# Optimization experiments

Measured on AMD Instinct MI355X. Metric: run time of the kernel, lower is better.

## Reference

```python
import jax, jax.numpy as jnp
import numpy as np

N_NODES = 100000


def gcn_conv(x, W, b, src, dst, n_nodes):
    """PyG-style GCNConv: out = D^{-1/2} (A + I) D^{-1/2} (x @ W) + b."""
    h = x @ W  # [N, F_out] transform first (smaller message dim)
    # add self-loops
    loops = jnp.arange(n_nodes, dtype=src.dtype)
    s = jnp.concatenate([src, loops])
    d = jnp.concatenate([dst, loops])
    # symmetric normalization
    deg = jnp.zeros((n_nodes,), dtype=h.dtype).at[d].add(1.0)
    dinv = jnp.where(deg > 0, jax.lax.rsqrt(deg), 0.0)
    norm = dinv[s] * dinv[d]  # [E+N]
    msg = h[s] * norm[:, None]  # gather from sources
    out = jax.ops.segment_sum(msg, d, num_segments=n_nodes)  # scatter-add at targets
    return out + b


def setup_inputs() -> dict:
    key = jax.random.key(0)
    k1, k2, k3, k4 = jax.random.split(key, 4)
    in_ch, hid, out_ch = 128, 75, 40
    n_edges = 3200000
    x = jax.random.normal(k1, (N_NODES, in_ch), dtype=jnp.float32)
    edge_index = jax.random.randint(k2, (2, n_edges), 0, N_NODES, dtype=jnp.int64)
    # Glorot-style init for GCNConv weights, zero bias (PyG default)
    W1 = jax.random.normal(k3, (in_ch, hid), dtype=jnp.float32) * (1.0 / np.sqrt(in_ch))
    b1 = jnp.zeros((hid,), dtype=jnp.float32)
    W2 = jax.random.normal(k4, (hid, out_ch), dtype=jnp.float32) * (1.0 / np.sqrt(hid))
    b2 = jnp.zeros((out_ch,), dtype=jnp.float32)
    return {"x": x, "edge_index": edge_index, "W1": W1, "b1": b1, "W2": W2, "b2": b2}


def reference(x, edge_index, W1, b1, W2, b2):
    src, dst = edge_index[0], edge_index[1]
    h = gcn_conv(x, W1, b1, src, dst, N_NODES)
    h = jax.nn.relu(h)
    h = gcn_conv(h, W2, b2, src, dst, N_NODES)
    return jax.nn.log_softmax(h, axis=1)
```

## Files before the change

### kernel.cpp

```cpp
#include <hip/hip_runtime.h>

#define N_NODES 100000
#define IN_CH 128
#define HID 75
#define OUT_CH 40
#define N_EDGES 3200000

#define NB 196
#define CAP 20000
#define EPT 16
#define PA_EDGES (EPT * 256)

typedef unsigned short u16;
typedef unsigned int u32;
typedef unsigned char u8;
typedef short short8 __attribute__((ext_vector_type(8)));
typedef float f32x4 __attribute__((ext_vector_type(4)));
typedef float f32x2 __attribute__((ext_vector_type(2)));
typedef u32 u32x2 __attribute__((ext_vector_type(2)));
typedef u32 u32x4 __attribute__((ext_vector_type(4)));

__device__ __forceinline__ u16 f2bf(float f) {
    u32 b = __float_as_uint(f);
    b += 0x7FFF + ((b >> 16) & 1);
    return (u16)(b >> 16);
}

#if __has_builtin(__builtin_amdgcn_cvt_pk_f32_fp8) && __has_builtin(__builtin_amdgcn_cvt_pk_fp8_f32)
#define HW_FP8 1
#else
#define HW_FP8 0
#endif

__device__ __forceinline__ float dec1_sw(u32 v) {
    u32 s = (v & 0x80u) << 24;
    u32 em = v & 0x7Fu;
    float mag = (em >= 8u) ? __uint_as_float((em << 20) + (120u << 23))
                           : (float)em * 0.001953125f;
    return __uint_as_float(s | __float_as_uint(mag));
}
template <int HI>
__device__ __forceinline__ f32x2 dec2(u32 w) {
#if HW_FP8
    return __builtin_amdgcn_cvt_pk_f32_fp8(w, HI);
#else
    f32x2 r;
    r.x = dec1_sw((w >> (HI * 16)) & 0xFFu);
    r.y = dec1_sw((w >> (HI * 16 + 8)) & 0xFFu);
    return r;
#endif
}
__device__ __forceinline__ u32 enc1(float f) {
#if HW_FP8
    return __builtin_amdgcn_cvt_pk_fp8_f32(f, f, 0u, false) & 0xFFu;
#else
    float cf = fminf(fmaxf(f, -448.f), 448.f);
    u32 b = __float_as_uint(cf);
    u32 sign = (b >> 24) & 0x80u;
    float af = fabsf(cf);
    if (af < 0.015625f) {
        u32 d = (u32)__builtin_rintf(af * 512.f);
        return sign | d;
    }
    u32 e = (b >> 23) & 0xFFu;
    u32 m = b & 0x7FFFFFu;
    u32 m8 = m >> 20;
    u32 rem = m & 0xFFFFFu;
    m8 += (rem > 0x80000u) || (rem == 0x80000u && (m8 & 1u));
    u32 ee = e - 120u;
    if (m8 == 8u) { m8 = 0u; ee += 1u; }
    if (ee > 15u || (ee == 15u && m8 == 7u)) { ee = 15u; m8 = 6u; }
    return sign | (ee << 3) | m8;
#endif
}

__global__ void probe64(const int* __restrict__ e, int* __restrict__ flag) {
    __shared__ int nonzero;
    if (threadIdx.x == 0) nonzero = 0;
    __syncthreads();
    int idx = threadIdx.x * 12497;
    if (e[2 * idx + 1] != 0) nonzero = 1;
    __syncthreads();
    if (threadIdx.x == 0) *flag = (nonzero == 0) ? 1 : 0;
}

__global__ __launch_bounds__(256) void init_misc(int* __restrict__ bucketCursor,
        u32* __restrict__ h1b32) {
    int i = blockIdx.x * 256 + threadIdx.x;
    if (i < NB * 16) bucketCursor[i] = 0;
    if (i < 800000) {
        int node = i >> 3, q = i & 7;
        h1b32[node * 48 + 40 + q] = 0;
    }
}

__global__ __launch_bounds__(256) void passA(const int* __restrict__ e,
        const int* __restrict__ flag, int* __restrict__ bucketCursor,
        unsigned* __restrict__ bucketBuf) {
    __shared__ int cnt[NB];
    __shared__ int base[NB];
    int t = threadIdx.x;
    for (int i = t; i < NB; i += 256) cnt[i] = 0;
    __syncthreads();
    bool w64 = (*flag != 0);
    int s_[EPT], d_[EPT];
    int eb = blockIdx.x * PA_EDGES + t;
#pragma unroll
    for (int k = 0; k < EPT; ++k) {
        int idx = eb + k * 256;
        int s = 0, d = -1;
        if (idx < N_EDGES) {
            if (w64) { s = e[2 * idx]; d = e[2 * (N_EDGES + idx)]; }
            else     { s = e[idx];     d = e[N_EDGES + idx]; }
            atomicAdd(&cnt[d >> 9], 1);
        }
        s_[k] = s; d_[k] = d;
    }
    __syncthreads();
    for (int i = t; i < NB; i += 256) {
        int c = cnt[i];
        base[i] = (c > 0) ? atomicAdd(&bucketCursor[i * 16], c) : 0;
        cnt[i] = 0;
    }
    __syncthreads();
#pragma unroll
    for (int k = 0; k < EPT; ++k) {
        int d = d_[k];
        if (d >= 0) {
            int b = d >> 9;
            int off = atomicAdd(&cnt[b], 1);
            int pos = base[b] + off;
            if (pos < CAP)
                bucketBuf[(size_t)b * CAP + pos] =
                    ((unsigned)(d & 511) << 17) | (unsigned)s_[k];
        }
    }
}

__global__ __launch_bounds__(256) void scan196(const int* __restrict__ bucketCursor,
        int* __restrict__ bucketStart, int* __restrict__ rowStart) {
    __shared__ int a[256], b[256];
    int t = threadIdx.x;
    int v = (t < NB) ? bucketCursor[t * 16] : 0;
    a[t] = v;
    __syncthreads();
    int* pin = a; int* pout = b;
    for (int o = 1; o < 256; o <<= 1) {
        int nv = pin[t] + ((t >= o) ? pin[t - o] : 0);
        pout[t] = nv;
        __syncthreads();
        int* tmp = pin; pin = pout; pout = tmp;
    }
    if (t < NB) bucketStart[t] = pin[t] - v;
    if (t == 0) rowStart[N_NODES] = N_EDGES;
}

__global__ __launch_bounds__(1024) void passB(const unsigned* __restrict__ bucketBuf,
        const int* __restrict__ bucketCursor, const int* __restrict__ bucketStart,
        int* __restrict__ csrSrc, int* __restrict__ rowStart, float* __restrict__ dinv) {
    __shared__ int cnt[512];
    __shared__ int sa[512], sb[512];
    int b = blockIdx.x;
    int t = threadIdx.x;
    int n = bucketCursor[b * 16];
    int start = bucketStart[b];
    if (t < 512) cnt[t] = 0;
    __syncthreads();
    const unsigned* buf = bucketBuf + (size_t)b * CAP;
    for (int i = t; i < n; i += 1024) atomicAdd(&cnt[buf[i] >> 17], 1);
    __syncthreads();
    if (t < 512) sa[t] = cnt[t];
    __syncthreads();
    int* pin = sa; int* pout = sb;
    for (int o = 1; o < 512; o <<= 1) {
        if (t < 512) pout[t] = pin[t] + ((t >= o) ? pin[t - o] : 0);
        __syncthreads();
        int* tmp = pin; pin = pout; pout = tmp;
    }
    int excl = 0;
    if (t < 512) {
        int deg = cnt[t];
        excl = pin[t] - deg;
        int node = b * 512 + t;
        if (node < N_NODES) {
            rowStart[node] = start + excl;
            dinv[node] = rsqrtf((float)deg + 1.0f);
        }
    }
    __syncthreads();
    if (t < 512) cnt[t] = excl;
    __syncthreads();
    for (int i = t; i < n; i += 1024) {
        unsigned p = buf[i];
        int pos = atomicAdd(&cnt[p >> 17], 1);
        csrSrc[start + pos] = (int)(p & 0x1FFFF);
    }
}

__global__ __launch_bounds__(256) void prep_w(const float* __restrict__ W1,
        const float* __restrict__ W2, u16* __restrict__ w1t, u16* __restrict__ w2t) {
    int g = blockIdx.x * 256 + threadIdx.x;
    int stride = gridDim.x * 256;
    for (int i = g; i < 80 * 128; i += stride) {
        int c = i >> 7, k = i & 127;
        w1t[i] = (c < HID) ? f2bf(W1[k * HID + c]) : (u16)0;
    }
    for (int i = g; i < 48 * 96; i += stride) {
        int c = i / 96, k = i - c * 96;
        w2t[i] = (c < OUT_CH && k < HID) ? f2bf(W2[k * OUT_CH + c]) : (u16)0;
    }
}

__global__ __launch_bounds__(256) void gemm1_mfma(const float* __restrict__ x,
        const u16* __restrict__ w1t, const float* __restrict__ dinv,
        u8* __restrict__ hsA8, u8* __restrict__ hsB8) {
    __shared__ u16 Wl[80 * 136];
    int t = threadIdx.x;
    {
        const u32* ws = (const u32*)w1t;
        u32* wd = (u32*)Wl;
        for (int i = t; i < 80 * 64; i += 256) {
            int r = i >> 6, c = i & 63;
            wd[r * 68 + c] = ws[i];
        }
    }
    __syncthreads();
    int wid = t >> 6, lane = t & 63;
    int bl = lane & 15, kh = lane >> 4;
    int row0 = blockIdx.x * 64 + wid * 16;
    short8 bf[5][4];
#pragma unroll
    for (int ct = 0; ct < 5; ++ct)
#pragma unroll
        for (int ks = 0; ks < 4; ++ks)
            bf[ct][ks] = *(const short8*)&Wl[(ct * 16 + bl) * 136 + ks * 32 + kh * 8];
    f32x4 zero = {0.f, 0.f, 0.f, 0.f};
    f32x4 acc[5];
#pragma unroll
    for (int ct = 0; ct < 5; ++ct) acc[ct] = zero;
    int arow = row0 + bl;
    bool av = (arow < N_NODES);
    const float* xr = x + (size_t)arow * IN_CH + kh * 8;
#pragma unroll
    for (int ks = 0; ks < 4; ++ks) {
        short8 af = {0, 0, 0, 0, 0, 0, 0, 0};
        if (av) {
            float4 lo = *(const float4*)(xr + ks * 32);
            float4 hi = *(const float4*)(xr + ks * 32 + 4);
            af[0] = (short)f2bf(lo.x); af[1] = (short)f2bf(lo.y);
            af[2] = (short)f2bf(lo.z); af[3] = (short)f2bf(lo.w);
            af[4] = (short)f2bf(hi.x); af[5] = (short)f2bf(hi.y);
            af[6] = (short)f2bf(hi.z); af[7] = (short)f2bf(hi.w);
        }
#pragma unroll
        for (int ct = 0; ct < 5; ++ct)
            acc[ct] = __builtin_amdgcn_mfma_f32_16x16x32_bf16(af, bf[ct][ks], acc[ct], 0, 0, 0);
    }
    int orow = row0 + kh * 4;
    float dn[4];
#pragma unroll
    for (int i = 0; i < 4; ++i)
        dn[i] = (orow + i < N_NODES) ? dinv[orow + i] * 8.f : 0.f;
#pragma unroll
    for (int ct = 0; ct < 5; ++ct) {
        int col = ct * 16 + bl;
#pragma unroll
        for (int i = 0; i < 4; ++i) {
            int r = orow + i;
            if (r < N_NODES) {
                u8 q8 = (u8)enc1(acc[ct][i] * dn[i]);
                if (ct < 4) hsA8[(size_t)r * 64 + col] = q8;
                else        hsB8[(size_t)r * 16 + (col - 64)] = q8;
            }
        }
    }
}

__global__ __launch_bounds__(256) void gemm2_mfma(const u16* __restrict__ h1b,
        const u16* __restrict__ w2t, const float* __restrict__ dinv,
        u8* __restrict__ hs2P) {
    __shared__ u16 Wl[48 * 104];
    int t = threadIdx.x;
    {
        const u32* ws = (const u32*)w2t;
        u32* wd = (u32*)Wl;
        for (int i = t; i < 48 * 48; i += 256) {
            int r = i / 48, c = i - r * 48;
            wd[r * 52 + c] = ws[i];
        }
    }
    __syncthreads();
    int wid = t >> 6, lane = t & 63;
    int bl = lane & 15, kh = lane >> 4;
    int row0 = blockIdx.x * 64 + wid * 16;
    short8 bf[3][3];
#pragma unroll
    for (int ct = 0; ct < 3; ++ct)
#pragma unroll
        for (int ks = 0; ks < 3; ++ks)
            bf[ct][ks] = *(const short8*)&Wl[(ct * 16 + bl) * 104 + ks * 32 + kh * 8];
    f32x4 zero = {0.f, 0.f, 0.f, 0.f};
    f32x4 acc[3];
#pragma unroll
    for (int ct = 0; ct < 3; ++ct) acc[ct] = zero;
    int arow = row0 + bl;
    bool av = (arow < N_NODES);
    const u16* hr = h1b + (size_t)arow * 96 + kh * 8;
#pragma unroll
    for (int ks = 0; ks < 3; ++ks) {
        short8 af = {0, 0, 0, 0, 0, 0, 0, 0};
        if (av) af = *(const short8*)(hr + ks * 32);
#pragma unroll
        for (int ct = 0; ct < 3; ++ct)
            acc[ct] = __builtin_amdgcn_mfma_f32_16x16x32_bf16(af, bf[ct][ks], acc[ct], 0, 0, 0);
    }
    int orow = row0 + kh * 4;
    float dn[4];
#pragma unroll
    for (int i = 0; i < 4; ++i)
        dn[i] = (orow + i < N_NODES) ? dinv[orow + i] * 8.f : 0.f;
#pragma unroll
    for (int ct = 0; ct < 3; ++ct) {
        int col = ct * 16 + bl;
#pragma unroll
        for (int i = 0; i < 4; ++i) {
            int r = orow + i;
            if (r < N_NODES && (ct < 2 || bl < 8)) {
                u8 q8 = (u8)enc1(acc[ct][i] * dn[i]);
                hs2P[(size_t)r * 64 + col] = q8;
            }
        }
    }
}

__global__ __launch_bounds__(256) void aggregate1(
        const char* __restrict__ tab, int delta1,
        const int* __restrict__ rowStart, const int* __restrict__ csrSrc,
        const float* __restrict__ dinv, const float* __restrict__ bias,
        u32* __restrict__ out) {
    int wid = threadIdx.x >> 6, lane = threadIdx.x & 63;
    int node = __builtin_amdgcn_readfirstlane(blockIdx.x * 4 + wid);
    if (node >= N_NODES) return;
    int g = lane / 5;
    int ll = lane - 5 * g;
    bool isB = (ll == 4);
    u32 loff = isB ? (u32)delta1 : (u32)ll * 16;
    int sh = isB ? 4 : 6;
    bool act = lane < 60;
    f32x2 acc[8];
#pragma unroll
    for (int k = 0; k < 8; ++k) { acc[k].x = 0.f; acc[k].y = 0.f; }
    if (lane < 5) {
        u32x4 v = *(const u32x4*)(tab + (((u32)node << sh) + loff));
        acc[0] += dec2<0>(v.x); acc[1] += dec2<1>(v.x);
        acc[2] += dec2<0>(v.y); acc[3] += dec2<1>(v.y);
        acc[4] += dec2<0>(v.z); acc[5] += dec2<1>(v.z);
        acc[6] += dec2<0>(v.w); acc[7] += dec2<1>(v.w);
    }
    int j = rowStart[node], end = rowStart[node + 1];
    for (; j + 24 <= end; j += 24) {
        u32 iv[2]; u32x4 vv[2];
#pragma unroll
        for (int q = 0; q < 2; ++q) iv[q] = act ? (u32)csrSrc[j + 12 * q + g] : 0u;
#pragma unroll
        for (int q = 0; q < 2; ++q) {
            u32x4 z = {0u, 0u, 0u, 0u};
            vv[q] = act ? *(const u32x4*)(tab + ((iv[q] << sh) + loff)) : z;
        }
#pragma unroll
        for (int q = 0; q < 2; ++q) {
            acc[0] += dec2<0>(vv[q].x); acc[1] += dec2<1>(vv[q].x);
            acc[2] += dec2<0>(vv[q].y); acc[3] += dec2<1>(vv[q].y);
            acc[4] += dec2<0>(vv[q].z); acc[5] += dec2<1>(vv[q].z);
            acc[6] += dec2<0>(vv[q].w); acc[7] += dec2<1>(vv[q].w);
        }
    }
    for (; j < end; j += 12) {
        bool p = act && (j + g < end);
        u32 ivx = p ? (u32)csrSrc[j + g] : 0u;
        u32x4 z = {0u, 0u, 0u, 0u};
        u32x4 v = p ? *(const u32x4*)(tab + ((ivx << sh) + loff)) : z;
        acc[0] += dec2<0>(v.x); acc[1] += dec2<1>(v.x);
        acc[2] += dec2<0>(v.y); acc[3] += dec2<1>(v.y);
        acc[4] += dec2<0>(v.z); acc[5] += dec2<1>(v.z);
        acc[6] += dec2<0>(v.w); acc[7] += dec2<1>(v.w);
    }
    float tt[16];
#pragma unroll
    for (int k = 0; k < 8; ++k) { tt[2 * k] = acc[k].x; tt[2 * k + 1] = acc[k].y; }
#pragma unroll
    for (int k = 0; k < 16; ++k) {
        tt[k] += __shfl(tt[k], lane + 30);
        tt[k] += __shfl(tt[k], lane + 10) + __shfl(tt[k], lane + 20);
        tt[k] += __shfl(tt[k], lane + 5);
    }
    if (lane < 5) {
        float dns = dinv[node] * 0.125f;
        u32x4 o0, o1;
#pragma unroll
        for (int k = 0; k < 8; ++k) {
            int f0 = 16 * lane + 2 * k;
            float rlo = (f0 < HID) ? fmaxf(fmaf(dns, tt[2 * k], bias[f0]), 0.f) : 0.f;
            float rhi = (f0 + 1 < HID) ? fmaxf(fmaf(dns, tt[2 * k + 1], bias[f0 + 1]), 0.f) : 0.f;
            u32 wd = ((u32)f2bf(rhi) << 16) | (u32)f2bf(rlo);
            if (k < 4) o0[k] = wd; else o1[k - 4] = wd;
        }
        *(u32x4*)(out + (size_t)node * 48 + 8 * lane) = o0;
        *(u32x4*)(out + (size_t)node * 48 + 8 * lane + 4) = o1;
    }
}

__global__ __launch_bounds__(256) void aggregate2(
        const char* __restrict__ tab,
        const int* __restrict__ rowStart, const int* __restrict__ csrSrc,
        const float* __restrict__ dinv, const float* __restrict__ bias,
        float* __restrict__ out) {
    int wid = threadIdx.x >> 6, lane = threadIdx.x & 63;
    int node = __builtin_amdgcn_readfirstlane(blockIdx.x * 4 + wid);
    if (node >= N_NODES) return;
    int g = lane / 5;
    int ll = lane - 5 * g;
    u32 loff = (u32)ll * 8;
    bool act = lane < 60;
    f32x2 a0 = {0.f, 0.f}, a1 = {0.f, 0.f}, a2 = {0.f, 0.f}, a3 = {0.f, 0.f};
    if (lane < 5) {
        u32x2 v = *(const u32x2*)(tab + (((u32)node << 6) + loff));
        a0 += dec2<0>(v.x); a1 += dec2<1>(v.x);
        a2 += dec2<0>(v.y); a3 += dec2<1>(v.y);
    }
    int j = rowStart[node], end = rowStart[node + 1];
    for (; j + 24 <= end; j += 24) {
        u32 iv[2]; u32x2 vv[2];
#pragma unroll
        for (int q = 0; q < 2; ++q) iv[q] = act ? (u32)csrSrc[j + 12 * q + g] : 0u;
#pragma unroll
        for (int q = 0; q < 2; ++q) {
            u32x2 z = {0u, 0u};
            vv[q] = act ? *(const u32x2*)(tab + ((iv[q] << 6) + loff)) : z;
        }
#pragma unroll
        for (int q = 0; q < 2; ++q) {
            a0 += dec2<0>(vv[q].x); a1 += dec2<1>(vv[q].x);
            a2 += dec2<0>(vv[q].y); a3 += dec2<1>(vv[q].y);
        }
    }
    for (; j < end; j += 12) {
        bool p = act && (j + g < end);
        u32 ivx = p ? (u32)csrSrc[j + g] : 0u;
        u32x2 z = {0u, 0u};
        u32x2 v = p ? *(const u32x2*)(tab + ((ivx << 6) + loff)) : z;
        a0 += dec2<0>(v.x); a1 += dec2<1>(v.x);
        a2 += dec2<0>(v.y); a3 += dec2<1>(v.y);
    }
    float tt[8] = {a0.x, a0.y, a1.x, a1.y, a2.x, a2.y, a3.x, a3.y};
#pragma unroll
    for (int k = 0; k < 8; ++k) {
        tt[k] += __shfl(tt[k], lane + 30);
        tt[k] += __shfl(tt[k], lane + 10) + __shfl(tt[k], lane + 20);
        tt[k] += __shfl(tt[k], lane + 5);
    }
    bool act5 = lane < 5;
    float vk[8];
    float m = -3.4e38f;
    if (act5) {
        float dns = dinv[node] * 0.125f;
#pragma unroll
        for (int k = 0; k < 8; ++k) {
            vk[k] = fmaf(dns, tt[k], bias[8 * ll + k]);
            m = fmaxf(m, vk[k]);
        }
    }
#pragma unroll
    for (int o = 1; o < 8; o <<= 1) m = fmaxf(m, __shfl_xor(m, o));
    float e = 0.f;
    if (act5) {
#pragma unroll
        for (int k = 0; k < 8; ++k) e += expf(vk[k] - m);
    }
#pragma unroll
    for (int o = 1; o < 8; o <<= 1) e += __shfl_xor(e, o);
    float lse = logf(e);
    if (act5) {
        float4 r0 = make_float4(vk[0] - m - lse, vk[1] - m - lse,
                                vk[2] - m - lse, vk[3] - m - lse);
        float4 r1 = make_float4(vk[4] - m - lse, vk[5] - m - lse,
                                vk[6] - m - lse, vk[7] - m - lse);
        *(float4*)(out + (size_t)node * OUT_CH + 8 * ll) = r0;
        *(float4*)(out + (size_t)node * OUT_CH + 8 * ll + 4) = r1;
    }
}

extern "C" void kernel_launch(void* const* d_in, const int* in_sizes, int n_in,
                              void* d_out, int out_size, void* d_ws, size_t ws_size,
                              hipStream_t stream) {
    const float* x  = (const float*)d_in[0];
    const int*   e  = (const int*)d_in[1];
    const float* W1 = (const float*)d_in[2];
    const float* b1 = (const float*)d_in[3];
    const float* W2 = (const float*)d_in[4];
    const float* b2 = (const float*)d_in[5];
    float* out = (float*)d_out;

    char* w = (char*)d_ws;
    u8* hsA8 = (u8*)w;
    u8* hsB8 = (u8*)(w + 6402048);
    unsigned* bucketBuf = (unsigned*)w;
    w += 15680000;
    u16* h1b  = (u16*)w; w += (size_t)100032 * 96 * 2;
    int* csrSrc = (int*)w; w += (size_t)N_EDGES * 4;
    u8* hs2P = (u8*)w; w += (size_t)100032 * 64;
    int* rowStart = (int*)w; w += 400016;
    float* dinv   = (float*)w; w += 400000;
    int* bucketCursor = (int*)w; w += NB * 16 * 4;
    int* bucketStart  = (int*)w; w += 1024;
    u16* w1t = (u16*)w; w += 80 * 128 * 2;
    u16* w2t = (u16*)w; w += 48 * 96 * 2;
    int* flag = (int*)w; w += 16;

    int delta1 = (int)((char*)hsB8 - (char*)hsA8);

    probe64<<<1, 256, 0, stream>>>(e, flag);
    init_misc<<<3126, 256, 0, stream>>>(bucketCursor, (u32*)h1b);
    passA<<<(N_EDGES + PA_EDGES - 1) / PA_EDGES, 256, 0, stream>>>(
        e, flag, bucketCursor, bucketBuf);
    scan196<<<1, 256, 0, stream>>>(bucketCursor, bucketStart, rowStart);
    passB<<<NB, 1024, 0, stream>>>(bucketBuf, bucketCursor, bucketStart,
                                   csrSrc, rowStart, dinv);
    prep_w<<<16, 256, 0, stream>>>(W1, W2, w1t, w2t);

    gemm1_mfma<<<(N_NODES + 63) / 64, 256, 0, stream>>>(x, w1t, dinv, hsA8, hsB8);
    aggregate1<<<(N_NODES + 3) / 4, 256, 0, stream>>>(
        (const char*)hsA8, delta1, rowStart, csrSrc, dinv, b1, (u32*)h1b);
    gemm2_mfma<<<(N_NODES + 63) / 64, 256, 0, stream>>>(h1b, w2t, dinv, hs2P);
    aggregate2<<<(N_NODES + 3) / 4, 256, 0, stream>>>(
        (const char*)hs2P, rowStart, csrSrc, dinv, b2, out);
}
```

Before: 257.6 us.

## Pack multiple degree-sorted nodes per wavefront in aggregation kernels

Builds a degree histogram and counting-sort permutation of nodes, then changes both aggregation kernels so each wavefront handles 12 (layer 1) or 8 (layer 2) nodes. Each node gets its own lane group that walks that node's edge list serially, instead of one node per wave with lanes split across edges. This removes the cross-lane shuffle reductions and the idle lanes on low-degree nodes. Sorting by degree balances the loop trip counts inside a wave. The cost is three extra small kernels with global atomics, scattered perm indirection, and serial per-lane edge loops whose gathers may have less memory-level parallelism.

```diff
diff --git a/kernel.cpp b/kernel.cpp
--- a/kernel.cpp
+++ b/kernel.cpp
@@ -19,6 +19,7 @@
 typedef float f32x2 __attribute__((ext_vector_type(2)));
 typedef u32 u32x2 __attribute__((ext_vector_type(2)));
 typedef u32 u32x4 __attribute__((ext_vector_type(4)));
+typedef u32x4 u32x4u __attribute__((aligned(4)));
 
 __device__ __forceinline__ u16 f2bf(float f) {
     u32 b = __float_as_uint(f);
@@ -85,9 +86,10 @@
 }
 
 __global__ __launch_bounds__(256) void init_misc(int* __restrict__ bucketCursor,
-        u32* __restrict__ h1b32) {
+        int* __restrict__ degHist, u32* __restrict__ h1b32) {
     int i = blockIdx.x * 256 + threadIdx.x;
     if (i < NB * 16) bucketCursor[i] = 0;
+    if (i < 256) degHist[i] = 0;
     if (i < 800000) {
         int node = i >> 3, q = i & 7;
         h1b32[node * 48 + 40 + q] = 0;
@@ -194,6 +196,41 @@
         unsigned p = buf[i];
         int pos = atomicAdd(&cnt[p >> 17], 1);
         csrSrc[start + pos] = (int)(p & 0x1FFFF);
+    }
+}
+
+__global__ __launch_bounds__(256) void hist_deg(const int* __restrict__ rowStart,
+        int* __restrict__ degHist) {
+    int i = blockIdx.x * 256 + threadIdx.x;
+    if (i < N_NODES) {
+        int deg = rowStart[i + 1] - rowStart[i];
+        atomicAdd(&degHist[min(deg, 255)], 1);
+    }
+}
+__global__ __launch_bounds__(256) void scan_bins(const int* __restrict__ degHist,
+        int* __restrict__ binCursor) {
+    __shared__ int a[256], b[256];
+    int t = threadIdx.x;
+    int v = degHist[t];
+    a[t] = v;
+    __syncthreads();
+    int* pin = a; int* pout = b;
+    for (int o = 1; o < 256; o <<= 1) {
+        pout[t] = pin[t] + ((t >= o) ? pin[t - o] : 0);
+        __syncthreads();
+        int* tmp = pin; pin = pout; pout = tmp;
+    }
+    binCursor[t] = pin[t] - v;
+}
+__global__ __launch_bounds__(256) void scatter_perm(const int* __restrict__ rowStart,
+        int* __restrict__ binCursor, int* __restrict__ perm) {
+    int i = blockIdx.x * 256 + threadIdx.x;
+    if (i < N_NODES) {
+        int deg = rowStart[i + 1] - rowStart[i];
+        int pos = atomicAdd(&binCursor[min(deg, 255)], 1);
+        perm[pos] = i;
+    } else if (i < 100032) {
+        perm[i] = N_NODES;
     }
 }
 
@@ -336,130 +373,103 @@
 __global__ __launch_bounds__(256) void aggregate1(
         const char* __restrict__ tab, int delta1,
         const int* __restrict__ rowStart, const int* __restrict__ csrSrc,
-        const float* __restrict__ dinv, const float* __restrict__ bias,
-        u32* __restrict__ out) {
+        const int* __restrict__ perm, const float* __restrict__ dinv,
+        const float* __restrict__ bias, u32* __restrict__ out) {
     int wid = threadIdx.x >> 6, lane = threadIdx.x & 63;
-    int node = __builtin_amdgcn_readfirstlane(blockIdx.x * 4 + wid);
-    if (node >= N_NODES) return;
     int g = lane / 5;
     int ll = lane - 5 * g;
+    bool glane = (g < 12);
+    int slot = (blockIdx.x * 4 + wid) * 12 + (glane ? g : 0);
+    int node = perm[slot];
+    bool valid = glane && (node < N_NODES);
+    int vnode = valid ? node : 0;
+    int rs = rowStart[vnode];
+    int end = valid ? rowStart[vnode + 1] : rs;
     bool isB = (ll == 4);
     u32 loff = isB ? (u32)delta1 : (u32)ll * 16;
     int sh = isB ? 4 : 6;
-    bool act = lane < 60;
     f32x2 acc[8];
 #pragma unroll
     for (int k = 0; k < 8; ++k) { acc[k].x = 0.f; acc[k].y = 0.f; }
-    if (lane < 5) {
-        u32x4 v = *(const u32x4*)(tab + (((u32)node << sh) + loff));
+    if (valid) {
+        u32x4 v = *(const u32x4*)(tab + (((u32)vnode << sh) + loff));
         acc[0] += dec2<0>(v.x); acc[1] += dec2<1>(v.x);
         acc[2] += dec2<0>(v.y); acc[3] += dec2<1>(v.y);
         acc[4] += dec2<0>(v.z); acc[5] += dec2<1>(v.z);
         acc[6] += dec2<0>(v.w); acc[7] += dec2<1>(v.w);
     }
-    int j = rowStart[node], end = rowStart[node + 1];
-    for (; j + 24 <= end; j += 24) {
-        u32 iv[2]; u32x4 vv[2];
-#pragma unroll
-        for (int q = 0; q < 2; ++q) iv[q] = act ? (u32)csrSrc[j + 12 * q + g] : 0u;
-#pragma unroll
-        for (int q = 0; q < 2; ++q) {
-            u32x4 z = {0u, 0u, 0u, 0u};
-            vv[q] = act ? *(const u32x4*)(tab + ((iv[q] << sh) + loff)) : z;
-        }
-#pragma unroll
-        for (int q = 0; q < 2; ++q) {
-            acc[0] += dec2<0>(vv[q].x); acc[1] += dec2<1>(vv[q].x);
-            acc[2] += dec2<0>(vv[q].y); acc[3] += dec2<1>(vv[q].y);
-            acc[4] += dec2<0>(vv[q].z); acc[5] += dec2<1>(vv[q].z);
-            acc[6] += dec2<0>(vv[q].w); acc[7] += dec2<1>(vv[q].w);
-        }
-    }
-    for (; j < end; j += 12) {
-        bool p = act && (j + g < end);
-        u32 ivx = p ? (u32)csrSrc[j + g] : 0u;
-        u32x4 z = {0u, 0u, 0u, 0u};
-        u32x4 v = p ? *(const u32x4*)(tab + ((ivx << sh) + loff)) : z;
+    int j = rs;
+    for (; j + 4 <= end; j += 4) {
+        u32x4 i4 = *(const u32x4u*)(csrSrc + j);
+#pragma unroll
+        for (int q = 0; q < 4; ++q) {
+            u32x4 v = *(const u32x4*)(tab + ((i4[q] << sh) + loff));
+            acc[0] += dec2<0>(v.x); acc[1] += dec2<1>(v.x);
+            acc[2] += dec2<0>(v.y); acc[3] += dec2<1>(v.y);
+            acc[4] += dec2<0>(v.z); acc[5] += dec2<1>(v.z);
+            acc[6] += dec2<0>(v.w); acc[7] += dec2<1>(v.w);
+        }
+    }
+    for (; j < end; ++j) {
+        u32 idx = (u32)csrSrc[j];
+        u32x4 v = *(const u32x4*)(tab + ((idx << sh) + loff));
         acc[0] += dec2<0>(v.x); acc[1] += dec2<1>(v.x);
         acc[2] += dec2<0>(v.y); acc[3] += dec2<1>(v.y);
         acc[4] += dec2<0>(v.z); acc[5] += dec2<1>(v.z);
         acc[6] += dec2<0>(v.w); acc[7] += dec2<1>(v.w);
     }
-    float tt[16];
-#pragma unroll
-    for (int k = 0; k < 8; ++k) { tt[2 * k] = acc[k].x; tt[2 * k + 1] = acc[k].y; }
-#pragma unroll
-    for (int k = 0; k < 16; ++k) {
-        tt[k] += __shfl(tt[k], lane + 30);
-        tt[k] += __shfl(tt[k], lane + 10) + __shfl(tt[k], lane + 20);
-        tt[k] += __shfl(tt[k], lane + 5);
-    }
-    if (lane < 5) {
-        float dns = dinv[node] * 0.125f;
+    if (valid) {
+        float dns = dinv[vnode] * 0.125f;
         u32x4 o0, o1;
 #pragma unroll
         for (int k = 0; k < 8; ++k) {
-            int f0 = 16 * lane + 2 * k;
-            float rlo = (f0 < HID) ? fmaxf(fmaf(dns, tt[2 * k], bias[f0]), 0.f) : 0.f;
-            float rhi = (f0 + 1 < HID) ? fmaxf(fmaf(dns, tt[2 * k + 1], bias[f0 + 1]), 0.f) : 0.f;
+            int f0 = 16 * ll + 2 * k;
+            float rlo = (f0 < HID) ? fmaxf(fmaf(dns, acc[k].x, bias[f0]), 0.f) : 0.f;
+            float rhi = (f0 + 1 < HID) ? fmaxf(fmaf(dns, acc[k].y, bias[f0 + 1]), 0.f) : 0.f;
             u32 wd = ((u32)f2bf(rhi) << 16) | (u32)f2bf(rlo);
             if (k < 4) o0[k] = wd; else o1[k - 4] = wd;
         }
-        *(u32x4*)(out + (size_t)node * 48 + 8 * lane) = o0;
-        *(u32x4*)(out + (size_t)node * 48 + 8 * lane + 4) = o1;
+        *(u32x4*)(out + (size_t)vnode * 48 + 8 * ll) = o0;
+        *(u32x4*)(out + (size_t)vnode * 48 + 8 * ll + 4) = o1;
     }
 }
 
 __global__ __launch_bounds__(256) void aggregate2(
         const char* __restrict__ tab,
         const int* __restrict__ rowStart, const int* __restrict__ csrSrc,
-        const float* __restrict__ dinv, const float* __restrict__ bias,
-        float* __restrict__ out) {
+        const int* __restrict__ perm, const float* __restrict__ dinv,
+        const float* __restrict__ bias, float* __restrict__ out) {
     int wid = threadIdx.x >> 6, lane = threadIdx.x & 63;
-    int node = __builtin_amdgcn_readfirstlane(blockIdx.x * 4 + wid);
-    if (node >= N_NODES) return;
-    int g = lane / 5;
-    int ll = lane - 5 * g;
+    int g = lane >> 3, ll = lane & 7;
+    int slot = (blockIdx.x * 4 + wid) * 8 + g;
+    int node = perm[slot];
+    int rs = rowStart[node];
+    int end = rowStart[node + 1];
     u32 loff = (u32)ll * 8;
-    bool act = lane < 60;
     f32x2 a0 = {0.f, 0.f}, a1 = {0.f, 0.f}, a2 = {0.f, 0.f}, a3 = {0.f, 0.f};
-    if (lane < 5) {
+    {
         u32x2 v = *(const u32x2*)(tab + (((u32)node << 6) + loff));
         a0 += dec2<0>(v.x); a1 += dec2<1>(v.x);
         a2 += dec2<0>(v.y); a3 += dec2<1>(v.y);
     }
-    int j = rowStart[node], end = rowStart[node + 1];
-    for (; j + 24 <= end; j += 24) {
-        u32 iv[2]; u32x2 vv[2];
-#pragma unroll
-        for (int q = 0; q < 2; ++q) iv[q] = act ? (u32)csrSrc[j + 12 * q + g] : 0u;
-#pragma unroll
-        for (int q = 0; q < 2; ++q) {
-            u32x2 z = {0u, 0u};
-            vv[q] = act ? *(const u32x2*)(tab + ((iv[q] << 6) + loff)) : z;
-        }
-#pragma unroll
-        for (int q = 0; q < 2; ++q) {
-            a0 += dec2<0>(vv[q].x); a1 += dec2<1>(vv[q].x);
-            a2 += dec2<0>(vv[q].y); a3 += dec2<1>(vv[q].y);
-        }
-    }
-    for (; j < end; j += 12) {
-        bool p = act && (j + g < end);
-        u32 ivx = p ? (u32)csrSrc[j + g] : 0u;
-        u32x2 z = {0u, 0u};
-        u32x2 v = p ? *(const u32x2*)(tab + ((ivx << 6) + loff)) : z;
+    int j = rs;
+    for (; j + 4 <= end; j += 4) {
+        u32x4 i4 = *(const u32x4u*)(csrSrc + j);
+#pragma unroll
+        for (int q = 0; q < 4; ++q) {
+            u32x2 v = *(const u32x2*)(tab + ((i4[q] << 6) + loff));
+            a0 += dec2<0>(v.x); a1 += dec2<1>(v.x);
+            a2 += dec2<0>(v.y); a3 += dec2<1>(v.y);
+        }
+    }
+    for (; j < end; ++j) {
+        u32 idx = (u32)csrSrc[j];
+        u32x2 v = *(const u32x2*)(tab + ((idx << 6) + loff));
         a0 += dec2<0>(v.x); a1 += dec2<1>(v.x);
         a2 += dec2<0>(v.y); a3 += dec2<1>(v.y);
     }
     float tt[8] = {a0.x, a0.y, a1.x, a1.y, a2.x, a2.y, a3.x, a3.y};
-#pragma unroll
-    for (int k = 0; k < 8; ++k) {
-        tt[k] += __shfl(tt[k], lane + 30);
-        tt[k] += __shfl(tt[k], lane + 10) + __shfl(tt[k], lane + 20);
-        tt[k] += __shfl(tt[k], lane + 5);
-    }
-    bool act5 = lane < 5;
+    bool act5 = (ll < 5);
     float vk[8];
     float m = -3.4e38f;
     if (act5) {
@@ -511,8 +521,11 @@
     u8* hs2P = (u8*)w; w += (size_t)100032 * 64;
     int* rowStart = (int*)w; w += 400016;
     float* dinv   = (float*)w; w += 400000;
+    int* perm     = (int*)w; w += 400128;
     int* bucketCursor = (int*)w; w += NB * 16 * 4;
     int* bucketStart  = (int*)w; w += 1024;
+    int* degHist  = (int*)w; w += 1024;
+    int* binCursor= (int*)w; w += 1024;
     u16* w1t = (u16*)w; w += 80 * 128 * 2;
     u16* w2t = (u16*)w; w += 48 * 96 * 2;
     int* flag = (int*)w; w += 16;
@@ -520,18 +533,21 @@
     int delta1 = (int)((char*)hsB8 - (char*)hsA8);
 
     probe64<<<1, 256, 0, stream>>>(e, flag);
-    init_misc<<<3126, 256, 0, stream>>>(bucketCursor, (u32*)h1b);
+    init_misc<<<3126, 256, 0, stream>>>(bucketCursor, degHist, (u32*)h1b);
     passA<<<(N_EDGES + PA_EDGES - 1) / PA_EDGES, 256, 0, stream>>>(
         e, flag, bucketCursor, bucketBuf);
     scan196<<<1, 256, 0, stream>>>(bucketCursor, bucketStart, rowStart);
     passB<<<NB, 1024, 0, stream>>>(bucketBuf, bucketCursor, bucketStart,
                                    csrSrc, rowStart, dinv);
+    hist_deg<<<391, 256, 0, stream>>>(rowStart, degHist);
+    scan_bins<<<1, 256, 0, stream>>>(degHist, binCursor);
+    scatter_perm<<<391, 256, 0, stream>>>(rowStart, binCursor, perm);
     prep_w<<<16, 256, 0, stream>>>(W1, W2, w1t, w2t);
 
     gemm1_mfma<<<(N_NODES + 63) / 64, 256, 0, stream>>>(x, w1t, dinv, hsA8, hsB8);
-    aggregate1<<<(N_NODES + 3) / 4, 256, 0, stream>>>(
-        (const char*)hsA8, delta1, rowStart, csrSrc, dinv, b1, (u32*)h1b);
+    aggregate1<<<2084, 256, 0, stream>>>(
+        (const char*)hsA8, delta1, rowStart, csrSrc, perm, dinv, b1, (u32*)h1b);
     gemm2_mfma<<<(N_NODES + 63) / 64, 256, 0, stream>>>(h1b, w2t, dinv, hs2P);
-    aggregate2<<<(N_NODES + 3) / 4, 256, 0, stream>>>(
-        (const char*)hs2P, rowStart, csrSrc, dinv, b2, out);
-}
+    aggregate2<<<3125, 256, 0, stream>>>(
+        (const char*)hs2P, rowStart, csrSrc, perm, dinv, b2, out);
+}
```

Result: slower. 702.0 us (+172.5%).
